# Kernel tuning notes

Hardware: AMD Instinct MI355X
Metric: run time of the kernel (lower is better)

Reference implementation:

```python
import jax, jax.numpy as jnp
import numpy as np

B, N, D_IN, D_OUT = 8, 2048, 256, 256
BN_EPS = 1e-5
SELU_ALPHA = 1.6732632423543772
SELU_SCALE = 1.0507009873554805


def setup_inputs() -> dict:
    key = jax.random.key(0)
    k1, k2, k3, k4 = jax.random.split(key, 4)
    lim_lin = 1.0 / np.sqrt(D_IN)
    return {
        "x": jax.random.normal(k1, (B, N, D_IN), dtype=jnp.float32),
        "w_map": jax.random.uniform(k2, (D_IN,), jnp.float32, -lim_lin, lim_lin),
        "w_att": jax.random.uniform(k3, (D_OUT, D_IN), jnp.float32, -lim_lin, lim_lin),
        "w_res": jax.random.uniform(k4, (D_OUT, D_IN), jnp.float32, -lim_lin, lim_lin),
        "gamma": jnp.ones((D_OUT,), jnp.float32),
        "beta": jnp.zeros((D_OUT,), jnp.float32),
    }


def _selu(x):
    x_clamped = jnp.clip(x, -10.0, 10.0)
    return SELU_SCALE * jnp.where(x > 0, x, SELU_ALPHA * (jnp.exp(x_clamped) - 1.0))


def reference(x, w_map, w_att, w_res, gamma, beta):
    # scores[b,i,j] = sum_d w_map[d] * x[b,i,d] * x[b,j,d]  (== W_map(x_i*x_j))
    scores = jnp.einsum("bid,bjd->bij", x * w_map, x)  # [B,N,N]
    attn = jax.nn.softmax(scores, axis=-1)
    aggregated = jnp.einsum("bij,bjd->bid", attn, x)  # [B,N,D]
    out = aggregated @ w_att.T + x @ w_res.T  # [B,N,D_OUT]
    # BatchNorm1d in training mode: stats over (batch, nodes) per channel, biased var
    mean = jnp.mean(out, axis=(0, 1))
    var = jnp.mean(jnp.square(out - mean), axis=(0, 1))
    out = (out - mean) * jax.lax.rsqrt(var + BN_EPS) * gamma + beta
    return _selu(out)
```

## Files before the change

### kernel.cpp

```cpp
#include <hip/hip_runtime.h>
#include <hip/hip_bf16.h>


typedef __attribute__((ext_vector_type(8))) short  bf16x8;
typedef __attribute__((ext_vector_type(4))) float  f32x4;

#define MFMA16(a, b, c) __builtin_amdgcn_mfma_f32_16x16x32_bf16((a), (b), (c), 0, 0, 0)

constexpr int   NB = 8, NN = 2048, ND = 256;
constexpr int   ROWS = NB * NN;
constexpr float BN_EPS = 1e-5f;
constexpr float SELU_ALPHA = 1.6732632423543772f;
constexpr float SELU_SCALE = 1.0507009873554805f;

__device__ __forceinline__ unsigned short f2bf(float f) {
  union { float f; unsigned int u; } v; v.f = f;
  unsigned int u = v.u;
  u += 0x7FFFu + ((u >> 16) & 1u);
  return (unsigned short)(u >> 16);
}
__device__ __forceinline__ float bf2f(unsigned short h) {
  union { float f; unsigned int u; } v; v.u = ((unsigned int)h) << 16;
  return v.f;
}

__device__ __forceinline__ void async_copy16(const unsigned short* g, unsigned short* l) {
  __builtin_amdgcn_global_load_lds(
      (const __attribute__((address_space(1))) void*)g,
      (__attribute__((address_space(3))) void*)l, 16, 0, 0);
}

__global__ __launch_bounds__(256) void k0_prep(const float* __restrict__ x,
                                               unsigned short* __restrict__ AX,
                                               unsigned short* __restrict__ Xt) {
  __shared__ unsigned short Ls[64 * 264];
  const int t = threadIdx.x;
  const int b = blockIdx.x & 7, rt = blockIdx.x >> 3;
  const int grb = b * NN + rt * 64;
  const int c = (t & 31) * 8, r0 = t >> 5;
#pragma unroll
  for (int q = 0; q < 8; ++q) {
    int r = r0 + q * 8;
    const float* xp = x + (size_t)(grb + r) * 256 + c;
    float4 a = *(const float4*)xp;
    float4 d = *(const float4*)(xp + 4);
    union { unsigned short s[8]; uint4 v; } xb;
    xb.s[0] = f2bf(a.x); xb.s[1] = f2bf(a.y); xb.s[2] = f2bf(a.z); xb.s[3] = f2bf(a.w);
    xb.s[4] = f2bf(d.x); xb.s[5] = f2bf(d.y); xb.s[6] = f2bf(d.z); xb.s[7] = f2bf(d.w);
    *(uint4*)(AX + (size_t)(grb + r) * 512 + 256 + c) = xb.v;
    *(uint4*)&Ls[r * 264 + c] = xb.v;
  }
  __syncthreads();
  unsigned short* dst = Xt + ((size_t)b * 256 + t) * 2048 + rt * 64;
#pragma unroll
  for (int k = 0; k < 8; ++k) {
    union { unsigned short s[8]; uint4 v; } o;
#pragma unroll
    for (int j = 0; j < 8; ++j) o.s[j] = Ls[(k * 8 + j) * 264 + t];
    *(uint4*)(dst + k * 8) = o.v;
  }
}

__global__ __launch_bounds__(256) void k0_wc(const float* __restrict__ w_att,
                                             const float* __restrict__ w_res,
                                             unsigned short* __restrict__ WC,
                                             float* __restrict__ sums) {
  if (blockIdx.x == 0 && threadIdx.x < 128)
    ((float4*)sums)[threadIdx.x] = make_float4(0.f, 0.f, 0.f, 0.f);
  int f = (blockIdx.x * 256 + threadIdx.x) * 8;
  int c = f >> 9, k = f & 511;
  const float* src = (k < 256) ? (w_att + c * 256 + k) : (w_res + c * 256 + (k - 256));
  float4 a = *(const float4*)src;
  float4 b = *(const float4*)(src + 4);
  union { unsigned short s[8]; uint4 v; } o;
  o.s[0] = f2bf(a.x); o.s[1] = f2bf(a.y); o.s[2] = f2bf(a.z); o.s[3] = f2bf(a.w);
  o.s[4] = f2bf(b.x); o.s[5] = f2bf(b.y); o.s[6] = f2bf(b.z); o.s[7] = f2bf(b.w);
  *(uint4*)(WC + f) = o.v;
}

__global__ __launch_bounds__(256, 1) void k1_attn(const float* __restrict__ w_map,
                                                  const unsigned short* AX,
                                                  const unsigned short* __restrict__ Xt,
                                                  unsigned short* AXw) {
  __shared__ unsigned short Ks[2][32 * 256];
  __shared__ unsigned short Vt[2][256 * 32];
  __shared__ unsigned short Psw[4][16 * 40];

  const int t = threadIdx.x;
  const int w = t >> 6, lane = t & 63, l15 = lane & 15, quad = lane >> 4;
  const int b = blockIdx.x & 7, it = blockIdx.x >> 3;
  const int gib = b * NN + it * 64;
  const unsigned short* Xtb = Xt + (size_t)b * 256 * 2048;
  const unsigned short* AXr = AX + (size_t)b * NN * 512 + 256;

  int ksOff[4], vtOff[4];
#pragma unroll
  for (int q = 0; q < 4; ++q) {
    int j = w * 8 + q * 2 + (lane >> 5);
    int ck = (lane & 31) ^ (j & 7);
    ksOff[q] = j * 512 + ck * 8;
    int d = w * 64 + q * 16 + (lane >> 2);
    int cv = (lane & 3) ^ ((d >> 1) & 3);
    vtOff[q] = d * 2048 + cv * 8;
  }
  const int ldsOff = w * 2048 + lane * 8;

  bf16x8 qf[8];
  {
    const unsigned short* xrow = AXr + (size_t)(it * 64 + w * 16 + l15) * 512;
#pragma unroll
    for (int kc = 0; kc < 8; ++kc) {
      bf16x8 xb = *(const bf16x8*)(xrow + kc * 32 + quad * 8);
      const float* wp = w_map + kc * 32 + quad * 8;
      float4 w0 = *(const float4*)wp, w1 = *(const float4*)(wp + 4);
      float wv[8] = {w0.x, w0.y, w0.z, w0.w, w1.x, w1.y, w1.z, w1.w};
      bf16x8 q;
#pragma unroll
      for (int i = 0; i < 8; ++i)
        q[i] = (short)f2bf(bf2f((unsigned short)xb[i]) * wv[i]);
      qf[kc] = q;
    }
  }

  const f32x4 fz = {0.f, 0.f, 0.f, 0.f};
  f32x4 oacc[16];
#pragma unroll
  for (int i = 0; i < 16; ++i) oacc[i] = fz;
  f32x4 oL = fz;

  bf16x8 onesFrag;
  {
    short o1 = (l15 == 0) ? (short)0x3F80 : (short)0;
#pragma unroll
    for (int i = 0; i < 8; ++i) onesFrag[i] = o1;
  }

#pragma unroll
  for (int q = 0; q < 4; ++q)
    async_copy16(AXr + ksOff[q], &Ks[0][ldsOff + q * 512]);
#pragma unroll
  for (int q = 0; q < 4; ++q)
    async_copy16(Xtb + vtOff[q], &Vt[0][ldsOff + q * 512]);

  for (int jt = 0; jt < 64; ++jt) {
    const int cur = jt & 1;
    __syncthreads();
    if (jt < 63) {
      const int jb = (jt + 1) * 32;
#pragma unroll
      for (int q = 0; q < 4; ++q)
        async_copy16(AXr + (size_t)jb * 512 + ksOff[q], &Ks[cur ^ 1][ldsOff + q * 512]);
#pragma unroll
      for (int q = 0; q < 4; ++q)
        async_copy16(Xtb + jb + vtOff[q], &Vt[cur ^ 1][ldsOff + q * 512]);
    }
#pragma unroll
    for (int jm = 0; jm < 2; ++jm) {
      const int j = jm * 16 + l15;
      f32x4 s = fz;
#pragma unroll
      for (int kc = 0; kc < 8; ++kc) {
        int ckk = kc * 4 + quad;
        bf16x8 kf = *(const bf16x8*)&Ks[cur][j * 256 + ((ckk ^ (j & 7)) * 8)];
        s = MFMA16(kf, qf[kc], s);
      }
      ushort4 pk;
      pk.x = f2bf(__expf(s[0])); pk.y = f2bf(__expf(s[1]));
      pk.z = f2bf(__expf(s[2])); pk.w = f2bf(__expf(s[3]));
      *(ushort4*)&Psw[w][l15 * 40 + jm * 16 + quad * 4] = pk;
    }
    bf16x8 af = *(const bf16x8*)&Psw[w][l15 * 40 + quad * 8];
#pragma unroll
    for (int nti = 0; nti < 16; ++nti) {
      const int d = nti * 16 + l15;
      bf16x8 vf = *(const bf16x8*)&Vt[cur][d * 32 + ((quad ^ ((d >> 1) & 3)) * 8)];
      oacc[nti] = MFMA16(af, vf, oacc[nti]);
    }
    oL = MFMA16(af, onesFrag, oL);
  }

  float li[4];
#pragma unroll
  for (int r = 0; r < 4; ++r)
    li[r] = 1.0f / __shfl(oL[r], lane & 48);
#pragma unroll
  for (int nti = 0; nti < 16; ++nti) {
    const int gcol = nti * 16 + l15;
#pragma unroll
    for (int r = 0; r < 4; ++r) {
      const int grow = gib + w * 16 + quad * 4 + r;
      AXw[(size_t)grow * 512 + gcol] = f2bf(oacc[nti][r] * li[r]);
    }
  }
}

__global__ __launch_bounds__(256, 2) void k2_gemm(const unsigned short* __restrict__ AX,
                                                  const unsigned short* __restrict__ WC,
                                                  float* __restrict__ out,
                                                  float* __restrict__ sums) {
  __shared__ unsigned short As[128 * 72];
  __shared__ unsigned short Bs[64 * 72];
  __shared__ float cs[64], cq[64];
  const int t = threadIdx.x;
  const int w = t >> 6, lane = t & 63, l15 = lane & 15, quad = lane >> 4;
  const int m0 = (blockIdx.x >> 2) * 128, n0 = (blockIdx.x & 3) * 64;
  if (t < 64) { cs[t] = 0.f; cq[t] = 0.f; }

  const f32x4 fz = {0.f, 0.f, 0.f, 0.f};
  f32x4 acc[4][2];
#pragma unroll
  for (int i = 0; i < 4; ++i) { acc[i][0] = fz; acc[i][1] = fz; }

  for (int kk = 0; kk < 512; kk += 64) {
    __syncthreads();
#pragma unroll
    for (int q = 0; q < 4; ++q) {
      int idx = t + q * 256;
      int row = idx >> 3, koff = (idx & 7) * 8;
      *(uint4*)&As[row * 72 + koff] = *(const uint4*)(AX + (size_t)(m0 + row) * 512 + kk + koff);
    }
#pragma unroll
    for (int q = 0; q < 2; ++q) {
      int idx = t + q * 256;
      int row = idx >> 3, koff = (idx & 7) * 8;
      *(uint4*)&Bs[row * 72 + koff] = *(const uint4*)(WC + (size_t)(n0 + row) * 512 + kk + koff);
    }
    __syncthreads();
#pragma unroll
    for (int kc = 0; kc < 2; ++kc) {
      bf16x8 b0 = *(const bf16x8*)&Bs[((w >> 1) * 32 + l15) * 72 + kc * 32 + quad * 8];
      bf16x8 b1 = *(const bf16x8*)&Bs[((w >> 1) * 32 + 16 + l15) * 72 + kc * 32 + quad * 8];
#pragma unroll
      for (int mt = 0; mt < 4; ++mt) {
        bf16x8 af = *(const bf16x8*)&As[((w & 1) * 64 + mt * 16 + l15) * 72 + kc * 32 + quad * 8];
        acc[mt][0] = MFMA16(af, b0, acc[mt][0]);
        acc[mt][1] = MFMA16(af, b1, acc[mt][1]);
      }
    }
  }
#pragma unroll
  for (int mt = 0; mt < 4; ++mt)
#pragma unroll
    for (int nt = 0; nt < 2; ++nt)
#pragma unroll
      for (int r = 0; r < 4; ++r) {
        int grow = m0 + (w & 1) * 64 + mt * 16 + quad * 4 + r;
        int gcol = n0 + (w >> 1) * 32 + nt * 16 + l15;
        out[(size_t)grow * 256 + gcol] = acc[mt][nt][r];
      }
#pragma unroll
  for (int nt = 0; nt < 2; ++nt) {
    float a = 0.f, b2 = 0.f;
#pragma unroll
    for (int mt = 0; mt < 4; ++mt)
#pragma unroll
      for (int r = 0; r < 4; ++r) {
        float v = acc[mt][nt][r];
        a += v; b2 += v * v;
      }
    a += __shfl_xor(a, 16);  a += __shfl_xor(a, 32);
    b2 += __shfl_xor(b2, 16); b2 += __shfl_xor(b2, 32);
    if (quad == 0) {
      int ci = (w >> 1) * 32 + nt * 16 + l15;
      atomicAdd(&cs[ci], a);
      atomicAdd(&cq[ci], b2);
    }
  }
  __syncthreads();
  if (t < 64) {
    atomicAdd(&sums[n0 + t], cs[t]);
    atomicAdd(&sums[256 + n0 + t], cq[t]);
  }
}

__global__ __launch_bounds__(256) void k4_bn_selu(float* __restrict__ out,
                                                  const float* __restrict__ sums,
                                                  const float* __restrict__ gamma,
                                                  const float* __restrict__ beta) {
  int f = (blockIdx.x * 256 + threadIdx.x) * 8;
  int c = f & 255;
  const float inv_m = 1.0f / 16384.0f;
  float4 v0 = *(const float4*)(out + f);
  float4 v1 = *(const float4*)(out + f + 4);
  float vv[8] = {v0.x, v0.y, v0.z, v0.w, v1.x, v1.y, v1.z, v1.w};
#pragma unroll
  for (int k = 0; k < 8; ++k) {
    int ch = c + k;
    float mean = sums[ch] * inv_m;
    float var = sums[256 + ch] * inv_m - mean * mean;
    float y = (vv[k] - mean) * rsqrtf(var + BN_EPS) * gamma[ch] + beta[ch];
    float yc = fminf(fmaxf(y, -10.f), 10.f);
    float r = (y > 0.f) ? y : (SELU_ALPHA * (expf(yc) - 1.0f));
    vv[k] = SELU_SCALE * r;
  }
  float4 o0 = {vv[0], vv[1], vv[2], vv[3]};
  float4 o1 = {vv[4], vv[5], vv[6], vv[7]};
  *(float4*)(out + f) = o0;
  *(float4*)(out + f + 4) = o1;
}

extern "C" void kernel_launch(void* const* d_in, const int* in_sizes, int n_in,
                              void* d_out, int out_size, void* d_ws, size_t ws_size,
                              hipStream_t stream) {
  const float* x     = (const float*)d_in[0];
  const float* w_map = (const float*)d_in[1];
  const float* w_att = (const float*)d_in[2];
  const float* w_res = (const float*)d_in[3];
  const float* gamma = (const float*)d_in[4];
  const float* beta  = (const float*)d_in[5];
  float* out = (float*)d_out;

  unsigned short* AX = (unsigned short*)d_ws;
  unsigned short* Xt = AX + (size_t)ROWS * 512;
  unsigned short* WC = Xt + (size_t)NB * 256 * 2048;
  float* sums = (float*)(WC + 256 * 512);

  k0_prep<<<256, 256, 0, stream>>>(x, AX, Xt);
  k0_wc<<<64, 256, 0, stream>>>(w_att, w_res, WC, sums);
  k1_attn<<<256, 256, 0, stream>>>(w_map, AX, Xt, AX);
  k2_gemm<<<512, 256, 0, stream>>>(AX, WC, out, sums);
  k4_bn_selu<<<2048, 256, 0, stream>>>(out, sums, gamma, beta);
}
```

Before: 185.5 us.

## Split attention key range across two warp groups with LDS reduction

The attention kernel now launches 512 threads per block. Two groups of four waves each process half of the key/value sequence (1024 keys) with their own double-buffered LDS tiles. At the end, group 1 writes its partial output accumulators and row sums to LDS, and group 0 adds them in, normalises and stores. This doubles the waves per block on a grid of only 256 blocks to improve latency hiding and CU utilisation. The cost is doubled LDS use per block, an extra reduction pass through shared memory, and higher register pressure under the 512-thread launch bound.

```diff
diff --git a/kernel.cpp b/kernel.cpp
--- a/kernel.cpp
+++ b/kernel.cpp
@@ -78,36 +78,38 @@
   *(uint4*)(WC + f) = o.v;
 }
 
-__global__ __launch_bounds__(256, 1) void k1_attn(const float* __restrict__ w_map,
+__global__ __launch_bounds__(512, 2) void k1_attn(const float* __restrict__ w_map,
                                                   const unsigned short* AX,
                                                   const unsigned short* __restrict__ Xt,
                                                   unsigned short* AXw) {
-  __shared__ unsigned short Ks[2][32 * 256];
-  __shared__ unsigned short Vt[2][256 * 32];
-  __shared__ unsigned short Psw[4][16 * 40];
+  __shared__ unsigned short Ks[2][2][32 * 256];
+  __shared__ unsigned short Vt[2][2][256 * 32];
+  __shared__ unsigned short Psw[8][16 * 40];
 
   const int t = threadIdx.x;
   const int w = t >> 6, lane = t & 63, l15 = lane & 15, quad = lane >> 4;
+  const int g = w >> 2, wg = w & 3;
   const int b = blockIdx.x & 7, it = blockIdx.x >> 3;
   const int gib = b * NN + it * 64;
   const unsigned short* Xtb = Xt + (size_t)b * 256 * 2048;
   const unsigned short* AXr = AX + (size_t)b * NN * 512 + 256;
+  const int jgbase = g * 1024;
 
   int ksOff[4], vtOff[4];
 #pragma unroll
   for (int q = 0; q < 4; ++q) {
-    int j = w * 8 + q * 2 + (lane >> 5);
+    int j = wg * 8 + q * 2 + (lane >> 5);
     int ck = (lane & 31) ^ (j & 7);
     ksOff[q] = j * 512 + ck * 8;
-    int d = w * 64 + q * 16 + (lane >> 2);
+    int d = wg * 64 + q * 16 + (lane >> 2);
     int cv = (lane & 3) ^ ((d >> 1) & 3);
     vtOff[q] = d * 2048 + cv * 8;
   }
-  const int ldsOff = w * 2048 + lane * 8;
+  const int ldsOff = wg * 2048 + lane * 8;
 
   bf16x8 qf[8];
   {
-    const unsigned short* xrow = AXr + (size_t)(it * 64 + w * 16 + l15) * 512;
+    const unsigned short* xrow = AXr + (size_t)(it * 64 + wg * 16 + l15) * 512;
 #pragma unroll
     for (int kc = 0; kc < 8; ++kc) {
       bf16x8 xb = *(const bf16x8*)(xrow + kc * 32 + quad * 8);
@@ -137,22 +139,22 @@
 
 #pragma unroll
   for (int q = 0; q < 4; ++q)
-    async_copy16(AXr + ksOff[q], &Ks[0][ldsOff + q * 512]);
+    async_copy16(AXr + (size_t)jgbase * 512 + ksOff[q], &Ks[g][0][ldsOff + q * 512]);
 #pragma unroll
   for (int q = 0; q < 4; ++q)
-    async_copy16(Xtb + vtOff[q], &Vt[0][ldsOff + q * 512]);
-
-  for (int jt = 0; jt < 64; ++jt) {
+    async_copy16(Xtb + jgbase + vtOff[q], &Vt[g][0][ldsOff + q * 512]);
+
+  for (int jt = 0; jt < 32; ++jt) {
     const int cur = jt & 1;
     __syncthreads();
-    if (jt < 63) {
-      const int jb = (jt + 1) * 32;
+    if (jt < 31) {
+      const int jb1 = jgbase + (jt + 1) * 32;
 #pragma unroll
       for (int q = 0; q < 4; ++q)
-        async_copy16(AXr + (size_t)jb * 512 + ksOff[q], &Ks[cur ^ 1][ldsOff + q * 512]);
+        async_copy16(AXr + (size_t)jb1 * 512 + ksOff[q], &Ks[g][cur ^ 1][ldsOff + q * 512]);
 #pragma unroll
       for (int q = 0; q < 4; ++q)
-        async_copy16(Xtb + jb + vtOff[q], &Vt[cur ^ 1][ldsOff + q * 512]);
+        async_copy16(Xtb + jb1 + vtOff[q], &Vt[g][cur ^ 1][ldsOff + q * 512]);
     }
 #pragma unroll
     for (int jm = 0; jm < 2; ++jm) {
@@ -161,7 +163,7 @@
 #pragma unroll
       for (int kc = 0; kc < 8; ++kc) {
         int ckk = kc * 4 + quad;
-        bf16x8 kf = *(const bf16x8*)&Ks[cur][j * 256 + ((ckk ^ (j & 7)) * 8)];
+        bf16x8 kf = *(const bf16x8*)&Ks[g][cur][j * 256 + ((ckk ^ (j & 7)) * 8)];
         s = MFMA16(kf, qf[kc], s);
       }
       ushort4 pk;
@@ -173,23 +175,52 @@
 #pragma unroll
     for (int nti = 0; nti < 16; ++nti) {
       const int d = nti * 16 + l15;
-      bf16x8 vf = *(const bf16x8*)&Vt[cur][d * 32 + ((quad ^ ((d >> 1) & 3)) * 8)];
+      bf16x8 vf = *(const bf16x8*)&Vt[g][cur][d * 32 + ((quad ^ ((d >> 1) & 3)) * 8)];
       oacc[nti] = MFMA16(af, vf, oacc[nti]);
     }
     oL = MFMA16(af, onesFrag, oL);
   }
 
-  float li[4];
-#pragma unroll
-  for (int r = 0; r < 4; ++r)
-    li[r] = 1.0f / __shfl(oL[r], lane & 48);
-#pragma unroll
-  for (int nti = 0; nti < 16; ++nti) {
-    const int gcol = nti * 16 + l15;
-#pragma unroll
-    for (int r = 0; r < 4; ++r) {
-      const int grow = gib + w * 16 + quad * 4 + r;
-      AXw[(size_t)grow * 512 + gcol] = f2bf(oacc[nti][r] * li[r]);
+  __syncthreads();
+  float* Obuf = (float*)&Ks[0][0][0];
+  float* Lb   = (float*)&Vt[0][0][0];
+  if (g == 1) {
+#pragma unroll
+    for (int nti = 0; nti < 16; ++nti)
+#pragma unroll
+      for (int r = 0; r < 4; ++r) {
+        int row = quad * 4 + r;
+        Obuf[wg * 4096 + row * 256 + (((nti + quad) & 15) << 4) + l15] = oacc[nti][r];
+      }
+    if (l15 == 0) {
+#pragma unroll
+      for (int r = 0; r < 4; ++r) Lb[wg * 16 + quad * 4 + r] = oL[r];
+    }
+  }
+  __syncthreads();
+  if (g == 0) {
+    float ls[4];
+#pragma unroll
+    for (int r = 0; r < 4; ++r) ls[r] = Lb[wg * 16 + quad * 4 + r];
+#pragma unroll
+    for (int nti = 0; nti < 16; ++nti)
+#pragma unroll
+      for (int r = 0; r < 4; ++r) {
+        int row = quad * 4 + r;
+        oacc[nti][r] += Obuf[wg * 4096 + row * 256 + (((nti + quad) & 15) << 4) + l15];
+      }
+    float li[4];
+#pragma unroll
+    for (int r = 0; r < 4; ++r)
+      li[r] = 1.0f / (__shfl(oL[r], lane & 48) + ls[r]);
+#pragma unroll
+    for (int nti = 0; nti < 16; ++nti) {
+      const int gcol = nti * 16 + l15;
+#pragma unroll
+      for (int r = 0; r < 4; ++r) {
+        const int grow = gib + wg * 16 + quad * 4 + r;
+        AXw[(size_t)grow * 512 + gcol] = f2bf(oacc[nti][r] * li[r]);
+      }
     }
   }
 }
@@ -317,7 +348,7 @@
 
   k0_prep<<<256, 256, 0, stream>>>(x, AX, Xt);
   k0_wc<<<64, 256, 0, stream>>>(w_att, w_res, WC, sums);
-  k1_attn<<<256, 256, 0, stream>>>(w_map, AX, Xt, AX);
+  k1_attn<<<256, 512, 0, stream>>>(w_map, AX, Xt, AX);
   k2_gemm<<<512, 256, 0, stream>>>(AX, WC, out, sums);
   k4_bn_selu<<<2048, 256, 0, stream>>>(out, sums, gamma, beta);
 }
```

Result: faster. 163.0 us (-12.1%).
